# Kernel optimization log

Measured on AMD Instinct MI355X. Metric: run time of the kernel, lower is better.

The kernel has to match this reference:

```python
import jax, jax.numpy as jnp
import numpy as np


def _dct1d_last(x, W_r, W_i):
    """DCT-II along last axis via the even/odd-reorder + FFT trick, ortho norm.

    x: [..., N] real. W_r/W_i: [1, N] rows = cos/sin(-k*pi/(2N)).
    """
    N = x.shape[-1]
    # v = [x[0], x[2], ...] ++ [x[N-1], x[N-3], ..., x[1]]  (torch index/inverted_index)
    v = jnp.concatenate([x[..., 0::2], x[..., 1::2][..., ::-1]], axis=-1)
    Vc = jnp.fft.fft(v, axis=-1)  # complex64
    V = Vc.real * W_r - Vc.imag * W_i  # [..., N]
    # ortho normalization: V[0] /= sqrt(N)*2 ; V[1:] /= sqrt(N/2)*2 ; then V *= 2
    s0 = 1.0 / (np.sqrt(N) * 2.0)
    s1 = 1.0 / (np.sqrt(N / 2.0) * 2.0)
    scale = jnp.concatenate([jnp.full((1,), s0, x.dtype), jnp.full((N - 1,), s1, x.dtype)])
    return 2.0 * V * scale


def setup_inputs() -> dict:
    key = jax.random.key(0)
    H, W = 512, 512
    x = jax.random.normal(key, (32, 3, H, W), dtype=jnp.float32)
    kw = -jnp.arange(W, dtype=jnp.float32)[None, :] * np.pi / (2 * W)
    kh = -jnp.arange(H, dtype=jnp.float32)[None, :] * np.pi / (2 * H)
    return {
        "x": x,
        "W_r_weight": jnp.cos(kw), "W_i_weight": jnp.sin(kw),
        "W_r_height": jnp.cos(kh), "W_i_height": jnp.sin(kh),
    }


def reference(x, W_r_weight, W_i_weight, W_r_height, W_i_height):
    # DCT along width (last axis)
    V = _dct1d_last(x, W_r_weight, W_i_weight)
    # transpose last two dims, DCT along height, transpose back
    V = jnp.swapaxes(V, -1, -2)
    V = _dct1d_last(V, W_r_height, W_i_height)
    return jnp.swapaxes(V, -1, -2)
```

## Files before the change

kernel.cpp:

```cpp
#include <hip/hip_runtime.h>
#include <math.h>

#define NN 512

typedef __attribute__((ext_vector_type(8))) short bf16x8;
typedef __attribute__((ext_vector_type(4))) float f32x4;
typedef __attribute__((ext_vector_type(4))) unsigned int u32x4;

__device__ inline unsigned short f2bf(float f) {
    unsigned u = __builtin_bit_cast(unsigned, f);
    u += 0x7fffu + ((u >> 16) & 1u);
    return (unsigned short)(u >> 16);
}
__device__ inline float bf2f(unsigned short h) {
    unsigned u = ((unsigned)h) << 16;
    return __builtin_bit_cast(float, u);
}
__device__ inline unsigned cvtpk_bf16(float lo, float hi) {
    unsigned r;
    asm("v_cvt_pk_bf16_f32 %0, %1, %2" : "=v"(r) : "v"(lo), "v"(hi));
    return r;
}

__global__ __launch_bounds__(256) void fill_dct_half(unsigned short* __restrict__ Ce,
                                                     unsigned short* __restrict__ Co) {
    int idx = blockIdx.x * 256 + threadIdx.x;
    int par = idx >> 16;
    int kk = (idx >> 8) & 255;
    int n = idx & 255;
    int k = 2 * kk + par;
    int m = ((2 * n + 1) * k) & 2047;
    float ang = (float)m * 3.0679615757712823e-3f;
    float s = (k == 0) ? 0.04419417382415922f : 0.0625f;
    unsigned short v = f2bf(s * cosf(ang));
    if (par) Co[kk * 256 + n] = v; else Ce[kk * 256 + n] = v;
}

#define GLB(p) ((const __attribute__((address_space(1))) unsigned int*)(const void*)(p))
#define LDS(p) ((__attribute__((address_space(3))) unsigned int*)(p))

template <int PASS>
__global__ __launch_bounds__(256, 2) void gemm_dct(const void* __restrict__ Ap,
                                                   const unsigned short* __restrict__ Ce,
                                                   const unsigned short* __restrict__ Cop,
                                                   void* __restrict__ Outp,
                                                   size_t strideIn, size_t strideOut) {
    const int nwg = (int)gridDim.x;
    const int cpx = nwg >> 3;
    const int bid = (int)blockIdx.x;
    const int nid = (bid & 7) * cpx + (bid >> 3);
    const int bx = nid & 3;
    const int by = (nid >> 2) & 3;
    const int bz = nid >> 4;

    __shared__ unsigned short sm[20480];
    unsigned short* const As = sm;
    unsigned short* const Bs = sm + (PASS == 1 ? 8192 : 12288);

    const int t = threadIdx.x;
    const int lane = t & 63;
    const int wave = t >> 6;
    const int wr = wave >> 1, wc = wave & 1;
    const int lr = lane & 15;
    const int kgx = ((lane >> 4) * 8) ^ (((lr >> 1) & 3) << 3);

    const int srow = t >> 2;
    const int sslot = t & 3;
    const int scol = (sslot ^ ((srow >> 1) & 3)) * 8;

    const int frow = t >> 1;
    const int fhalf = t & 1;
    const int fs0 = fhalf * 2;
    const int fxw = (frow >> 1) & 3;
    const int fslot0 = (fs0 ^ fxw) * 8;
    const int fslot1 = ((fs0 + 1) ^ fxw) * 8;

    const float* Xf = nullptr;
    const unsigned short* Tp = nullptr;
    const unsigned short* Gmat;
    int grow0, sgn, row0, col0;
    if constexpr (PASS == 1) {
        Xf = (const float*)Ap + (size_t)bz * strideIn;
        row0 = by * 128;
        col0 = bx * 128;
        Gmat = (bx < 2) ? Ce : Cop; grow0 = (bx & 1) * 128; sgn = (bx >= 2);
    } else {
        Tp = (const unsigned short*)Ap + (size_t)bz * strideIn;
        col0 = bx * 128;
        row0 = 0;
        Gmat = (by < 2) ? Ce : Cop; grow0 = (by & 1) * 128; sgn = (by >= 2);
    }
    const float sgnf = sgn ? -1.0f : 1.0f;

    f32x4 acc[4][4] = {};

    f32x4 rf0[4], rm0[4], rf1[4], rm1[4];
    bf16x8 gf0[2], gm0[2], gf1[2], gm1[2];

    auto stageG = [&](unsigned short* dst, int buf, int k0) {
        __builtin_amdgcn_global_load_lds(GLB(Gmat + (size_t)(grow0 + srow) * 256 + k0 + scol),
                                         LDS(&dst[buf * 4096 + srow * 32 + sslot * 8]), 16, 0, 0);
        __builtin_amdgcn_global_load_lds(GLB(Gmat + (size_t)(grow0 + 64 + srow) * 256 + k0 + scol),
                                         LDS(&dst[buf * 4096 + (64 + srow) * 32 + sslot * 8]), 16, 0, 0);
    };
    auto lr1 = [&](f32x4 (&rf)[4], f32x4 (&rm)[4], int k0) {
        const float* bfp = Xf + (size_t)(row0 + frow) * NN + k0 + fhalf * 16;
        const float* bmp = Xf + (size_t)(row0 + frow) * NN + (496 - k0 - fhalf * 16);
#pragma unroll
        for (int q = 0; q < 4; ++q) {
            rf[q] = *reinterpret_cast<const f32x4*>(bfp + 4 * q);
            rm[q] = *reinterpret_cast<const f32x4*>(bmp + 4 * q);
        }
    };
    auto cw1 = [&](f32x4 (&rf)[4], f32x4 (&rm)[4], int buf) {
        unsigned p[8];
#pragma unroll
        for (int q = 0; q < 8; ++q) {
            const int j0 = 2 * q, j1 = 2 * q + 1;
            const int r0 = 15 - j0, r1 = 15 - j1;
            float s0 = fmaf(sgnf, rm[r0 >> 2][r0 & 3], rf[j0 >> 2][j0 & 3]);
            float s1 = fmaf(sgnf, rm[r1 >> 2][r1 & 3], rf[j1 >> 2][j1 & 3]);
            p[q] = cvtpk_bf16(s0, s1);
        }
        u32x4 w0 = {p[0], p[1], p[2], p[3]};
        u32x4 w1 = {p[4], p[5], p[6], p[7]};
        *reinterpret_cast<u32x4*>(&As[buf * 4096 + frow * 32 + fslot0]) = w0;
        *reinterpret_cast<u32x4*>(&As[buf * 4096 + frow * 32 + fslot1]) = w1;
    };
    auto lr2 = [&](bf16x8 (&gf)[2], bf16x8 (&gm)[2], int k0) {
        const unsigned short* bfp = Tp + (size_t)(col0 + frow) * NN + k0 + fhalf * 16;
        const unsigned short* bmp = Tp + (size_t)(col0 + frow) * NN + (496 - k0 - fhalf * 16);
        gf[0] = *reinterpret_cast<const bf16x8*>(bfp);
        gf[1] = *reinterpret_cast<const bf16x8*>(bfp + 8);
        gm[0] = *reinterpret_cast<const bf16x8*>(bmp);
        gm[1] = *reinterpret_cast<const bf16x8*>(bmp + 8);
    };
    auto cw2 = [&](bf16x8 (&gf)[2], bf16x8 (&gm)[2], int buf) {
        unsigned p[8];
#pragma unroll
        for (int q = 0; q < 8; ++q) {
            const int j0 = 2 * q, j1 = 2 * q + 1;
            const int r0 = 15 - j0, r1 = 15 - j1;
            float a0 = bf2f((unsigned short)gf[j0 >> 3][j0 & 7]);
            float a1 = bf2f((unsigned short)gf[j1 >> 3][j1 & 7]);
            float b0 = bf2f((unsigned short)gm[r0 >> 3][r0 & 7]);
            float b1 = bf2f((unsigned short)gm[r1 >> 3][r1 & 7]);
            p[q] = cvtpk_bf16(fmaf(sgnf, b0, a0), fmaf(sgnf, b1, a1));
        }
        u32x4 w0 = {p[0], p[1], p[2], p[3]};
        u32x4 w1 = {p[4], p[5], p[6], p[7]};
        *reinterpret_cast<u32x4*>(&Bs[buf * 4096 + frow * 32 + fslot0]) = w0;
        *reinterpret_cast<u32x4*>(&Bs[buf * 4096 + frow * 32 + fslot1]) = w1;
    };
    auto compute = [&](int kt) {
        const int bA = (PASS == 1) ? (kt & 1) : (kt % 3);
        const int bB = (PASS == 1) ? (kt % 3) : (kt & 1);
        bf16x8 a[4], b[4];
#pragma unroll
        for (int mi = 0; mi < 4; ++mi)
            a[mi] = *reinterpret_cast<const bf16x8*>(
                &As[bA * 4096 + (wr * 64 + mi * 16 + lr) * 32 + kgx]);
#pragma unroll
        for (int ni = 0; ni < 4; ++ni)
            b[ni] = *reinterpret_cast<const bf16x8*>(
                &Bs[bB * 4096 + (wc * 64 + ni * 16 + lr) * 32 + kgx]);
        __builtin_amdgcn_s_setprio(1);
#pragma unroll
        for (int mi = 0; mi < 4; ++mi)
#pragma unroll
            for (int ni = 0; ni < 4; ++ni)
                acc[mi][ni] = __builtin_amdgcn_mfma_f32_16x16x32_bf16(a[mi], b[ni],
                                                                      acc[mi][ni], 0, 0, 0);
        __builtin_amdgcn_s_setprio(0);
    };

    if constexpr (PASS == 1) {
        stageG(Bs, 0, 0);
        lr1(rf0, rm0, 0);
        asm volatile("" ::: "memory");
        cw1(rf0, rm0, 0);
        stageG(Bs, 1, 32);
        asm volatile("" ::: "memory");
        lr1(rf1, rm1, 32);
        lr1(rf0, rm0, 64);
        asm volatile("s_waitcnt lgkmcnt(0)" ::: "memory");
        asm volatile("s_waitcnt vmcnt(18)" ::: "memory");
        __builtin_amdgcn_s_barrier();
    } else {
        stageG(As, 0, 0);
        lr2(gf0, gm0, 0);
        asm volatile("" ::: "memory");
        cw2(gf0, gm0, 0);
        stageG(As, 1, 32);
        asm volatile("" ::: "memory");
        lr2(gf1, gm1, 32);
        lr2(gf0, gm0, 64);
        asm volatile("s_waitcnt lgkmcnt(0)" ::: "memory");
        asm volatile("s_waitcnt vmcnt(10)" ::: "memory");
        __builtin_amdgcn_s_barrier();
    }

#pragma unroll
    for (int kt = 0; kt < 8; ++kt) {
        if (kt + 1 <= 7) {
            if constexpr (PASS == 1) {
                if ((kt + 1) & 1) cw1(rf1, rm1, 1); else cw1(rf0, rm0, 0);
            } else {
                if ((kt + 1) & 1) cw2(gf1, gm1, 1); else cw2(gf0, gm0, 0);
            }
        }
        if (kt + 2 <= 7)
            stageG(PASS == 1 ? Bs : As, (kt + 2) % 3, (kt + 2) * 32);
        asm volatile("" ::: "memory");
        if (kt + 3 <= 7) {
            if constexpr (PASS == 1) {
                if ((kt + 3) & 1) lr1(rf1, rm1, (kt + 3) * 32); else lr1(rf0, rm0, (kt + 3) * 32);
            } else {
                if ((kt + 3) & 1) lr2(gf1, gm1, (kt + 3) * 32); else lr2(gf0, gm0, (kt + 3) * 32);
            }
        }
        compute(kt);
        asm volatile("s_waitcnt lgkmcnt(0)" ::: "memory");
        if (kt <= 4) {
            if constexpr (PASS == 1) asm volatile("s_waitcnt vmcnt(18)" ::: "memory");
            else                     asm volatile("s_waitcnt vmcnt(10)" ::: "memory");
        } else if (kt == 5) {
            if constexpr (PASS == 1) asm volatile("s_waitcnt vmcnt(10)" ::: "memory");
            else                     asm volatile("s_waitcnt vmcnt(6)" ::: "memory");
        } else if (kt == 6) {
            asm volatile("s_waitcnt vmcnt(0)" ::: "memory");
        }
        if (kt < 7) __builtin_amdgcn_s_barrier();
    }

    if constexpr (PASS == 1) {
        unsigned short* T = (unsigned short*)Outp + (size_t)bz * strideOut;
        __syncthreads();
#pragma unroll
        for (int mi = 0; mi < 4; ++mi)
#pragma unroll
            for (int ni = 0; ni < 4; ++ni) {
                int gr = wr * 64 + mi * 16 + (lane >> 4) * 4;
                int gc = wc * 64 + ni * 16 + lr;
                ushort4 v;
                v.x = f2bf(acc[mi][ni][0]);
                v.y = f2bf(acc[mi][ni][1]);
                v.z = f2bf(acc[mi][ni][2]);
                v.w = f2bf(acc[mi][ni][3]);
                *reinterpret_cast<ushort4*>(&sm[gc * 132 + gr]) = v;
            }
        __syncthreads();
#pragma unroll
        for (int it = 0; it < 8; ++it) {
            int gcr = wave * 32 + it * 4 + (lane >> 4);
            int physRow = (bx & 1) * 256 + 2 * gcr + (bx >> 1);
            int cb = lr * 8;
            u32x4 d = *reinterpret_cast<const u32x4*>(&sm[gcr * 132 + cb]);
            *reinterpret_cast<u32x4*>(&T[(size_t)physRow * NN + row0 + cb]) = d;
        }
    } else {
        float* O = (float*)Outp + (size_t)bz * strideOut;
#pragma unroll
        for (int mi = 0; mi < 4; ++mi)
#pragma unroll
            for (int ni = 0; ni < 4; ++ni) {
                int gc = col0 + wc * 64 + ni * 16 + lr;
#pragma unroll
                for (int rr = 0; rr < 4; ++rr) {
                    int grl = wr * 64 + mi * 16 + (lane >> 4) * 4 + rr;
                    int ih = (by & 1) * 128 + grl;
                    int q = 2 * ih + (by >> 1);
                    O[(size_t)q * NN + gc] = acc[mi][ni][rr];
                }
            }
    }
}

extern "C" void kernel_launch(void* const* d_in, const int* in_sizes, int n_in,
                              void* d_out, int out_size, void* d_ws, size_t ws_size,
                              hipStream_t stream) {
    const float* x = (const float*)d_in[0];
    float* out = (float*)d_out;

    const int imgs = in_sizes[0] / (NN * NN);
    const size_t imgElems = (size_t)NN * NN;
    const size_t imgB16 = imgElems * 2;

    unsigned short* Ce = (unsigned short*)d_ws;
    unsigned short* Co = Ce + 65536;
    unsigned short* Tb = Co + 65536;

    long long budget = (long long)ws_size - 262144;
    int maxchunk = (int)(budget / (long long)imgB16);
    if (maxchunk < 1) maxchunk = 1;
    if (maxchunk > imgs) maxchunk = imgs;

    hipLaunchKernelGGL(fill_dct_half, dim3(512), dim3(256), 0, stream, Ce, Co);

    for (int i0 = 0; i0 < imgs; i0 += maxchunk) {
        int c = imgs - i0 < maxchunk ? imgs - i0 : maxchunk;
        hipLaunchKernelGGL((gemm_dct<1>), dim3(16 * c), dim3(256), 0, stream,
                           x + (size_t)i0 * imgElems, Ce, Co, Tb, imgElems, imgElems);
        hipLaunchKernelGGL((gemm_dct<2>), dim3(16 * c), dim3(256), 0, stream,
                           Tb, Ce, Co, out + (size_t)i0 * imgElems, imgElems, imgElems);
    }
}
```

Baseline: 78.48 us.

## Make GEMM DCT kernels persistent with cross-tile prefetch pipelining

Caps the grid at 512 blocks and lets each block process several consecutive tiles. The K-loop software pipeline now runs across tile boundaries, so the next tile's loads and staging are issued during the last iterations of the current tile. Pass 1 gets a separate epilogue LDS region so the prefetched buffers are not overwritten. This targets per-block prologue and epilogue bubbles and launch tail, at the cost of more LDS in pass 1, which may lower occupancy.

Result: slower. 112.2 us (+43.0%).

```diff
diff --git a/kernel.cpp b/kernel.cpp
--- a/kernel.cpp
+++ b/kernel.cpp
@@ -44,18 +44,23 @@
                                                    const unsigned short* __restrict__ Ce,
                                                    const unsigned short* __restrict__ Cop,
                                                    void* __restrict__ Outp,
-                                                   size_t strideIn, size_t strideOut) {
+                                                   size_t strideIn, size_t strideOut,
+                                                   int tiles, int tpb) {
     const int nwg = (int)gridDim.x;
     const int cpx = nwg >> 3;
     const int bid = (int)blockIdx.x;
-    const int nid = (bid & 7) * cpx + (bid >> 3);
-    const int bx = nid & 3;
-    const int by = (nid >> 2) & 3;
-    const int bz = nid >> 4;
-
-    __shared__ unsigned short sm[20480];
+    const int swzb = (bid & 7) * cpx + (bid >> 3);
+    const int first = swzb * tpb;
+    int nt = tiles - first;
+    if (nt > tpb) nt = tpb;
+    if (nt <= 0) return;
+
+    __shared__ unsigned short sm[PASS == 1 ? 37376 : 20480];
     unsigned short* const As = sm;
     unsigned short* const Bs = sm + (PASS == 1 ? 8192 : 12288);
+    unsigned short* const Rs = (PASS == 1) ? As : Bs;
+    unsigned short* const Gs = (PASS == 1) ? Bs : As;
+    unsigned short* const smE = sm + 20480;
 
     const int t = threadIdx.x;
     const int lane = t & 63;
@@ -75,67 +80,74 @@
     const int fslot0 = (fs0 ^ fxw) * 8;
     const int fslot1 = ((fs0 + 1) ^ fxw) * 8;
 
-    const float* Xf = nullptr;
-    const unsigned short* Tp = nullptr;
-    const unsigned short* Gmat;
-    int grow0, sgn, row0, col0;
-    if constexpr (PASS == 1) {
-        Xf = (const float*)Ap + (size_t)bz * strideIn;
-        row0 = by * 128;
-        col0 = bx * 128;
-        Gmat = (bx < 2) ? Ce : Cop; grow0 = (bx & 1) * 128; sgn = (bx >= 2);
-    } else {
-        Tp = (const unsigned short*)Ap + (size_t)bz * strideIn;
-        col0 = bx * 128;
-        row0 = 0;
-        Gmat = (by < 2) ? Ce : Cop; grow0 = (by & 1) * 128; sgn = (by >= 2);
-    }
-    const float sgnf = sgn ? -1.0f : 1.0f;
+    struct TileP {
+        const float* Xf;
+        const unsigned short* Tp;
+        const unsigned short* G;
+        float sgnf;
+        int grow0, row0, col0, bx, by, bz;
+    };
+    auto mk = [&](int nid) {
+        TileP P;
+        P.bx = nid & 3; P.by = (nid >> 2) & 3; P.bz = nid >> 4;
+        if constexpr (PASS == 1) {
+            P.Xf = (const float*)Ap + (size_t)P.bz * strideIn; P.Tp = nullptr;
+            P.row0 = P.by * 128; P.col0 = P.bx * 128;
+            P.G = (P.bx < 2) ? Ce : Cop; P.grow0 = (P.bx & 1) * 128;
+            P.sgnf = (P.bx >= 2) ? -1.0f : 1.0f;
+        } else {
+            P.Xf = nullptr; P.Tp = (const unsigned short*)Ap + (size_t)P.bz * strideIn;
+            P.col0 = P.bx * 128; P.row0 = 0;
+            P.G = (P.by < 2) ? Ce : Cop; P.grow0 = (P.by & 1) * 128;
+            P.sgnf = (P.by >= 2) ? -1.0f : 1.0f;
+        }
+        return P;
+    };
 
     f32x4 acc[4][4] = {};
 
     f32x4 rf0[4], rm0[4], rf1[4], rm1[4];
     bf16x8 gf0[2], gm0[2], gf1[2], gm1[2];
 
-    auto stageG = [&](unsigned short* dst, int buf, int k0) {
-        __builtin_amdgcn_global_load_lds(GLB(Gmat + (size_t)(grow0 + srow) * 256 + k0 + scol),
-                                         LDS(&dst[buf * 4096 + srow * 32 + sslot * 8]), 16, 0, 0);
-        __builtin_amdgcn_global_load_lds(GLB(Gmat + (size_t)(grow0 + 64 + srow) * 256 + k0 + scol),
-                                         LDS(&dst[buf * 4096 + (64 + srow) * 32 + sslot * 8]), 16, 0, 0);
-    };
-    auto lr1 = [&](f32x4 (&rf)[4], f32x4 (&rm)[4], int k0) {
-        const float* bfp = Xf + (size_t)(row0 + frow) * NN + k0 + fhalf * 16;
-        const float* bmp = Xf + (size_t)(row0 + frow) * NN + (496 - k0 - fhalf * 16);
+    auto stageG = [&](const TileP& P, int bofs, int k0) {
+        __builtin_amdgcn_global_load_lds(GLB(P.G + (size_t)(P.grow0 + srow) * 256 + k0 + scol),
+                                         LDS(&Gs[bofs + srow * 32 + sslot * 8]), 16, 0, 0);
+        __builtin_amdgcn_global_load_lds(GLB(P.G + (size_t)(P.grow0 + 64 + srow) * 256 + k0 + scol),
+                                         LDS(&Gs[bofs + (64 + srow) * 32 + sslot * 8]), 16, 0, 0);
+    };
+    auto lr1 = [&](const TileP& P, f32x4 (&rf)[4], f32x4 (&rm)[4], int k0) {
+        const float* bfp = P.Xf + (size_t)(P.row0 + frow) * NN + k0 + fhalf * 16;
+        const float* bmp = P.Xf + (size_t)(P.row0 + frow) * NN + (496 - k0 - fhalf * 16);
 #pragma unroll
         for (int q = 0; q < 4; ++q) {
             rf[q] = *reinterpret_cast<const f32x4*>(bfp + 4 * q);
             rm[q] = *reinterpret_cast<const f32x4*>(bmp + 4 * q);
         }
     };
-    auto cw1 = [&](f32x4 (&rf)[4], f32x4 (&rm)[4], int buf) {
+    auto cw1 = [&](const TileP& P, f32x4 (&rf)[4], f32x4 (&rm)[4], int bofs) {
         unsigned p[8];
 #pragma unroll
         for (int q = 0; q < 8; ++q) {
             const int j0 = 2 * q, j1 = 2 * q + 1;
             const int r0 = 15 - j0, r1 = 15 - j1;
-            float s0 = fmaf(sgnf, rm[r0 >> 2][r0 & 3], rf[j0 >> 2][j0 & 3]);
-            float s1 = fmaf(sgnf, rm[r1 >> 2][r1 & 3], rf[j1 >> 2][j1 & 3]);
+            float s0 = fmaf(P.sgnf, rm[r0 >> 2][r0 & 3], rf[j0 >> 2][j0 & 3]);
+            float s1 = fmaf(P.sgnf, rm[r1 >> 2][r1 & 3], rf[j1 >> 2][j1 & 3]);
             p[q] = cvtpk_bf16(s0, s1);
         }
         u32x4 w0 = {p[0], p[1], p[2], p[3]};
         u32x4 w1 = {p[4], p[5], p[6], p[7]};
-        *reinterpret_cast<u32x4*>(&As[buf * 4096 + frow * 32 + fslot0]) = w0;
-        *reinterpret_cast<u32x4*>(&As[buf * 4096 + frow * 32 + fslot1]) = w1;
-    };
-    auto lr2 = [&](bf16x8 (&gf)[2], bf16x8 (&gm)[2], int k0) {
-        const unsigned short* bfp = Tp + (size_t)(col0 + frow) * NN + k0 + fhalf * 16;
-        const unsigned short* bmp = Tp + (size_t)(col0 + frow) * NN + (496 - k0 - fhalf * 16);
+        *reinterpret_cast<u32x4*>(&Rs[bofs + frow * 32 + fslot0]) = w0;
+        *reinterpret_cast<u32x4*>(&Rs[bofs + frow * 32 + fslot1]) = w1;
+    };
+    auto lr2 = [&](const TileP& P, bf16x8 (&gf)[2], bf16x8 (&gm)[2], int k0) {
+        const unsigned short* bfp = P.Tp + (size_t)(P.col0 + frow) * NN + k0 + fhalf * 16;
+        const unsigned short* bmp = P.Tp + (size_t)(P.col0 + frow) * NN + (496 - k0 - fhalf * 16);
         gf[0] = *reinterpret_cast<const bf16x8*>(bfp);
         gf[1] = *reinterpret_cast<const bf16x8*>(bfp + 8);
         gm[0] = *reinterpret_cast<const bf16x8*>(bmp);
         gm[1] = *reinterpret_cast<const bf16x8*>(bmp + 8);
     };
-    auto cw2 = [&](bf16x8 (&gf)[2], bf16x8 (&gm)[2], int buf) {
+    auto cw2 = [&](const TileP& P, bf16x8 (&gf)[2], bf16x8 (&gm)[2], int bofs) {
         unsigned p[8];
 #pragma unroll
         for (int q = 0; q < 8; ++q) {
@@ -145,25 +157,25 @@
             float a1 = bf2f((unsigned short)gf[j1 >> 3][j1 & 7]);
             float b0 = bf2f((unsigned short)gm[r0 >> 3][r0 & 7]);
             float b1 = bf2f((unsigned short)gm[r1 >> 3][r1 & 7]);
-            p[q] = cvtpk_bf16(fmaf(sgnf, b0, a0), fmaf(sgnf, b1, a1));
+            p[q] = cvtpk_bf16(fmaf(P.sgnf, b0, a0), fmaf(P.sgnf, b1, a1));
         }
         u32x4 w0 = {p[0], p[1], p[2], p[3]};
         u32x4 w1 = {p[4], p[5], p[6], p[7]};
-        *reinterpret_cast<u32x4*>(&Bs[buf * 4096 + frow * 32 + fslot0]) = w0;
-        *reinterpret_cast<u32x4*>(&Bs[buf * 4096 + frow * 32 + fslot1]) = w1;
-    };
-    auto compute = [&](int kt) {
-        const int bA = (PASS == 1) ? (kt & 1) : (kt % 3);
-        const int bB = (PASS == 1) ? (kt % 3) : (kt & 1);
+        *reinterpret_cast<u32x4*>(&Rs[bofs + frow * 32 + fslot0]) = w0;
+        *reinterpret_cast<u32x4*>(&Rs[bofs + frow * 32 + fslot1]) = w1;
+    };
+    auto compute = [&](int rofs, int gofs) {
+        const int aofs = (PASS == 1) ? rofs : gofs;
+        const int bofs = (PASS == 1) ? gofs : rofs;
         bf16x8 a[4], b[4];
 #pragma unroll
         for (int mi = 0; mi < 4; ++mi)
             a[mi] = *reinterpret_cast<const bf16x8*>(
-                &As[bA * 4096 + (wr * 64 + mi * 16 + lr) * 32 + kgx]);
+                &As[aofs + (wr * 64 + mi * 16 + lr) * 32 + kgx]);
 #pragma unroll
         for (int ni = 0; ni < 4; ++ni)
             b[ni] = *reinterpret_cast<const bf16x8*>(
-                &Bs[bB * 4096 + (wc * 64 + ni * 16 + lr) * 32 + kgx]);
+                &Bs[bofs + (wc * 64 + ni * 16 + lr) * 32 + kgx]);
         __builtin_amdgcn_s_setprio(1);
 #pragma unroll
         for (int mi = 0; mi < 4; ++mi)
@@ -173,106 +185,118 @@
                                                                       acc[mi][ni], 0, 0, 0);
         __builtin_amdgcn_s_setprio(0);
     };
-
-    if constexpr (PASS == 1) {
-        stageG(Bs, 0, 0);
-        lr1(rf0, rm0, 0);
-        asm volatile("" ::: "memory");
-        cw1(rf0, rm0, 0);
-        stageG(Bs, 1, 32);
-        asm volatile("" ::: "memory");
-        lr1(rf1, rm1, 32);
-        lr1(rf0, rm0, 64);
-        asm volatile("s_waitcnt lgkmcnt(0)" ::: "memory");
-        asm volatile("s_waitcnt vmcnt(18)" ::: "memory");
-        __builtin_amdgcn_s_barrier();
-    } else {
-        stageG(As, 0, 0);
-        lr2(gf0, gm0, 0);
-        asm volatile("" ::: "memory");
-        cw2(gf0, gm0, 0);
-        stageG(As, 1, 32);
-        asm volatile("" ::: "memory");
-        lr2(gf1, gm1, 32);
-        lr2(gf0, gm0, 64);
-        asm volatile("s_waitcnt lgkmcnt(0)" ::: "memory");
-        asm volatile("s_waitcnt vmcnt(10)" ::: "memory");
-        __builtin_amdgcn_s_barrier();
-    }
-
-#pragma unroll
-    for (int kt = 0; kt < 8; ++kt) {
-        if (kt + 1 <= 7) {
-            if constexpr (PASS == 1) {
-                if ((kt + 1) & 1) cw1(rf1, rm1, 1); else cw1(rf0, rm0, 0);
-            } else {
-                if ((kt + 1) & 1) cw2(gf1, gm1, 1); else cw2(gf0, gm0, 0);
+    auto doLR = [&](const TileP& P, int s, int k0) {
+        if constexpr (PASS == 1) {
+            if (s & 1) lr1(P, rf1, rm1, k0); else lr1(P, rf0, rm0, k0);
+        } else {
+            if (s & 1) lr2(P, gf1, gm1, k0); else lr2(P, gf0, gm0, k0);
+        }
+    };
+    auto doCW = [&](const TileP& P, int s) {
+        const int bofs = (s & 1) * 4096;
+        if constexpr (PASS == 1) {
+            if (s & 1) cw1(P, rf1, rm1, bofs); else cw1(P, rf0, rm0, bofs);
+        } else {
+            if (s & 1) cw2(P, gf1, gm1, bofs); else cw2(P, gf0, gm0, bofs);
+        }
+    };
+
+    int c0 = 0, c1 = 4096, c2 = 8192;
+    auto gof = [&](int s) { int m = s % 3; return m == 0 ? c0 : (m == 1 ? c1 : c2); };
+
+    TileP P0 = mk(first);
+    TileP P1 = (nt > 1) ? mk(first + 1) : P0;
+
+    stageG(P0, c0, 0);
+    doLR(P0, 0, 0);
+    asm volatile("" ::: "memory");
+    doCW(P0, 0);
+    stageG(P0, c1, 32);
+    asm volatile("" ::: "memory");
+    doLR(P0, 1, 32);
+    doLR(P0, 2, 64);
+    asm volatile("s_waitcnt lgkmcnt(0)" ::: "memory");
+    if constexpr (PASS == 1) asm volatile("s_waitcnt vmcnt(18)" ::: "memory");
+    else                     asm volatile("s_waitcnt vmcnt(10)" ::: "memory");
+    __builtin_amdgcn_s_barrier();
+
+    for (int tt = 0; tt < nt; ++tt) {
+        const bool last = (tt == nt - 1);
+#pragma unroll
+        for (int kt = 0; kt < 8; ++kt) {
+            if (kt < 7)        doCW(P0, kt + 1);
+            else if (!last)    doCW(P1, 0);
+            if (kt < 6)        stageG(P0, gof(kt + 2), (kt + 2) * 32);
+            else if (!last)    stageG(P1, gof(kt + 2), (kt - 6) * 32);
+            asm volatile("" ::: "memory");
+            if (kt < 5)        doLR(P0, kt + 3, (kt + 3) * 32);
+            else if (!last)    doLR(P1, kt + 3, (kt - 5) * 32);
+            compute((kt & 1) * 4096, gof(kt));
+            asm volatile("s_waitcnt lgkmcnt(0)" ::: "memory");
+            if (!last || kt <= 4) {
+                if constexpr (PASS == 1) asm volatile("s_waitcnt vmcnt(18)" ::: "memory");
+                else                     asm volatile("s_waitcnt vmcnt(10)" ::: "memory");
+            } else if (kt == 5) {
+                if constexpr (PASS == 1) asm volatile("s_waitcnt vmcnt(10)" ::: "memory");
+                else                     asm volatile("s_waitcnt vmcnt(6)" ::: "memory");
+            } else if (kt == 6) {
+                asm volatile("s_waitcnt vmcnt(0)" ::: "memory");
             }
-        }
-        if (kt + 2 <= 7)
-            stageG(PASS == 1 ? Bs : As, (kt + 2) % 3, (kt + 2) * 32);
-        asm volatile("" ::: "memory");
-        if (kt + 3 <= 7) {
-            if constexpr (PASS == 1) {
-                if ((kt + 3) & 1) lr1(rf1, rm1, (kt + 3) * 32); else lr1(rf0, rm0, (kt + 3) * 32);
-            } else {
-                if ((kt + 3) & 1) lr2(gf1, gm1, (kt + 3) * 32); else lr2(gf0, gm0, (kt + 3) * 32);
+            if (kt < 7) __builtin_amdgcn_s_barrier();
+        }
+
+        if constexpr (PASS == 1) {
+            unsigned short* T = (unsigned short*)Outp + (size_t)P0.bz * strideOut;
+#pragma unroll
+            for (int mi = 0; mi < 4; ++mi)
+#pragma unroll
+                for (int ni = 0; ni < 4; ++ni) {
+                    int gr = wr * 64 + mi * 16 + (lane >> 4) * 4;
+                    int gc = wc * 64 + ni * 16 + lr;
+                    ushort4 v;
+                    v.x = f2bf(acc[mi][ni][0]);
+                    v.y = f2bf(acc[mi][ni][1]);
+                    v.z = f2bf(acc[mi][ni][2]);
+                    v.w = f2bf(acc[mi][ni][3]);
+                    *reinterpret_cast<ushort4*>(&smE[gc * 132 + gr]) = v;
+                }
+            asm volatile("s_waitcnt lgkmcnt(0)" ::: "memory");
+            __builtin_amdgcn_s_barrier();
+#pragma unroll
+            for (int it = 0; it < 8; ++it) {
+                int gcr = wave * 32 + it * 4 + (lane >> 4);
+                int physRow = (P0.bx & 1) * 256 + 2 * gcr + (P0.bx >> 1);
+                int cb = lr * 8;
+                u32x4 d = *reinterpret_cast<const u32x4*>(&smE[gcr * 132 + cb]);
+                *reinterpret_cast<u32x4*>(&T[(size_t)physRow * NN + P0.row0 + cb]) = d;
             }
-        }
-        compute(kt);
-        asm volatile("s_waitcnt lgkmcnt(0)" ::: "memory");
-        if (kt <= 4) {
-            if constexpr (PASS == 1) asm volatile("s_waitcnt vmcnt(18)" ::: "memory");
-            else                     asm volatile("s_waitcnt vmcnt(10)" ::: "memory");
-        } else if (kt == 5) {
-            if constexpr (PASS == 1) asm volatile("s_waitcnt vmcnt(10)" ::: "memory");
-            else                     asm volatile("s_waitcnt vmcnt(6)" ::: "memory");
-        } else if (kt == 6) {
-            asm volatile("s_waitcnt vmcnt(0)" ::: "memory");
-        }
-        if (kt < 7) __builtin_amdgcn_s_barrier();
-    }
-
-    if constexpr (PASS == 1) {
-        unsigned short* T = (unsigned short*)Outp + (size_t)bz * strideOut;
-        __syncthreads();
-#pragma unroll
-        for (int mi = 0; mi < 4; ++mi)
-#pragma unroll
-            for (int ni = 0; ni < 4; ++ni) {
-                int gr = wr * 64 + mi * 16 + (lane >> 4) * 4;
-                int gc = wc * 64 + ni * 16 + lr;
-                ushort4 v;
-                v.x = f2bf(acc[mi][ni][0]);
-                v.y = f2bf(acc[mi][ni][1]);
-                v.z = f2bf(acc[mi][ni][2]);
-                v.w = f2bf(acc[mi][ni][3]);
-                *reinterpret_cast<ushort4*>(&sm[gc * 132 + gr]) = v;
-            }
-        __syncthreads();
-#pragma unroll
-        for (int it = 0; it < 8; ++it) {
-            int gcr = wave * 32 + it * 4 + (lane >> 4);
-            int physRow = (bx & 1) * 256 + 2 * gcr + (bx >> 1);
-            int cb = lr * 8;
-            u32x4 d = *reinterpret_cast<const u32x4*>(&sm[gcr * 132 + cb]);
-            *reinterpret_cast<u32x4*>(&T[(size_t)physRow * NN + row0 + cb]) = d;
-        }
-    } else {
-        float* O = (float*)Outp + (size_t)bz * strideOut;
-#pragma unroll
-        for (int mi = 0; mi < 4; ++mi)
-#pragma unroll
-            for (int ni = 0; ni < 4; ++ni) {
-                int gc = col0 + wc * 64 + ni * 16 + lr;
-#pragma unroll
-                for (int rr = 0; rr < 4; ++rr) {
-                    int grl = wr * 64 + mi * 16 + (lane >> 4) * 4 + rr;
-                    int ih = (by & 1) * 128 + grl;
-                    int q = 2 * ih + (by >> 1);
-                    O[(size_t)q * NN + gc] = acc[mi][ni][rr];
+        } else {
+            __builtin_amdgcn_s_barrier();
+            float* O = (float*)Outp + (size_t)P0.bz * strideOut;
+#pragma unroll
+            for (int mi = 0; mi < 4; ++mi)
+#pragma unroll
+                for (int ni = 0; ni < 4; ++ni) {
+                    int gc = P0.col0 + wc * 64 + ni * 16 + lr;
+#pragma unroll
+                    for (int rr = 0; rr < 4; ++rr) {
+                        int grl = wr * 64 + mi * 16 + (lane >> 4) * 4 + rr;
+                        int ih = (P0.by & 1) * 128 + grl;
+                        int q = 2 * ih + (P0.by >> 1);
+                        O[(size_t)q * NN + gc] = acc[mi][ni][rr];
+                    }
                 }
-            }
+        }
+
+        if (!last) {
+#pragma unroll
+            for (int mi = 0; mi < 4; ++mi)
+#pragma unroll
+                for (int ni = 0; ni < 4; ++ni) acc[mi][ni] = f32x4{0.f, 0.f, 0.f, 0.f};
+            P0 = P1;
+            if (tt + 2 < nt) P1 = mk(first + tt + 2);
+            int tmpo = c2; c2 = c1; c1 = c0; c0 = tmpo;
+        }
     }
 }
 
@@ -299,9 +323,14 @@
 
     for (int i0 = 0; i0 < imgs; i0 += maxchunk) {
         int c = imgs - i0 < maxchunk ? imgs - i0 : maxchunk;
-        hipLaunchKernelGGL((gemm_dct<1>), dim3(16 * c), dim3(256), 0, stream,
-                           x + (size_t)i0 * imgElems, Ce, Co, Tb, imgElems, imgElems);
-        hipLaunchKernelGGL((gemm_dct<2>), dim3(16 * c), dim3(256), 0, stream,
-                           Tb, Ce, Co, out + (size_t)i0 * imgElems, imgElems, imgElems);
+        int tiles = 16 * c;
+        int blocks = tiles < 512 ? tiles : 512;
+        int tpb = (tiles + blocks - 1) / blocks;
+        hipLaunchKernelGGL((gemm_dct<1>), dim3(blocks), dim3(256), 0, stream,
+                           x + (size_t)i0 * imgElems, Ce, Co, Tb, imgElems, imgElems,
+                           tiles, tpb);
+        hipLaunchKernelGGL((gemm_dct<2>), dim3(blocks), dim3(256), 0, stream,
+                           Tb, Ce, Co, out + (size_t)i0 * imgElems, imgElems, imgElems,
+                           tiles, tpb);
     }
 }
```
